# Kernel optimization log

Measured on AMD Instinct MI355X. Metric: run time of the kernel, lower is better.

## Reference

```python
import jax, jax.numpy as jnp
import numpy as np

L = 2    # num_graph_layers
T = 16   # num_tasks (batch of episodes)
N = 128  # num_samples (nodes per episode)
F = 128  # num_node_feats
BN_EPS = 1e-5


def setup_inputs() -> dict:
    key = jax.random.key(0)
    ks = jax.random.split(key, 8)
    return {
        "node_feats": jax.random.normal(ks[0], (T, N, F), dtype=jnp.float32),
        "edge_feats": jax.random.uniform(ks[1], (T, N, N, F), dtype=jnp.float32),
        # Conv3d(3->1, 1x1x1) weight+bias per layer -> 3 scalars + 1 bias
        "edge_w": (jax.random.normal(ks[2], (L, 3), dtype=jnp.float32) * 0.5),
        "edge_b": (jax.random.normal(ks[3], (L,), dtype=jnp.float32) * 0.1),
        # Conv2d(2->1, 1x1, no bias) -> 2 scalars per layer
        "comb_w": (jax.random.normal(ks[4], (L, 2), dtype=jnp.float32) * 0.5),
        # Conv1d(F->F, k=1, no bias) -> [out,in] per layer
        "node_w": (jax.random.normal(ks[5], (L, F, F), dtype=jnp.float32) / np.sqrt(F).astype(np.float32)),
        # BatchNorm1d affine params
        "bn_gamma": jnp.ones((L, F), dtype=jnp.float32),
        "bn_beta": jnp.zeros((L, F), dtype=jnp.float32),
    }


def _lrelu(x):
    return jnp.where(x >= 0, x, 0.01 * x)  # torch LeakyReLU default slope


def _sim_cal(x):
    # x: [T,N,F] -> clamped [cos_sim, 1-cos_sim]: [T,2,N,N]
    g = jnp.einsum('tnf,tmf->tnm', x, x)
    nrm = jnp.linalg.norm(x, axis=-1)              # [T,N]
    denom = nrm[:, :, None] * nrm[:, None, :] + 1e-6
    sim = (g / denom)[:, None]                     # [T,1,N,N]
    pred = jnp.concatenate([sim, 1.0 - sim], axis=1)
    return jnp.clip(pred, 0.0, 1.0)


def reference(node_feats, edge_feats, edge_w, edge_b, comb_w, node_w, bn_gamma, bn_beta):
    outs = [_sim_cal(node_feats)]
    n = node_feats.shape[1]
    diag_mask = (1.0 - jnp.eye(n, dtype=node_feats.dtype))[None, :, :, None]  # [1,N,N,1]
    for l in range(L):
        x = node_feats                                     # [T,N,F]
        # --- EdgeUpdateNetwork: Conv3d(3->1,1x1x1) over channels [x_i, x_i-x_j, edge] + tanh ---
        diff = x[:, :, None, :] - x[:, None, :, :]         # [T,N,N,F]
        xi = jnp.broadcast_to(x[:, :, None, :], diff.shape)
        e = jnp.tanh(edge_w[l, 0] * xi + edge_w[l, 1] * diff
                     + edge_w[l, 2] * edge_feats + edge_b[l])
        edge_feats = e * diag_mask                         # zero diagonal
        # --- NodeUpdateNetwork ---
        aggr = edge_feats.sum(axis=2)                      # [T,N,F]
        h = _lrelu(comb_w[l, 0] * x + comb_w[l, 1] * aggr) # Conv2d(2->1) + LeakyReLU
        y = jnp.einsum('tnf,gf->tng', h, node_w[l])        # Conv1d(F->F, k=1)
        mu = y.mean(axis=(0, 1))                           # BN over (batch, length)
        var = y.var(axis=(0, 1))
        y = (y - mu) * jax.lax.rsqrt(var + BN_EPS) * bn_gamma[l] + bn_beta[l]
        node_feats = _lrelu(y)
        outs.append(_sim_cal(node_feats))
    return tuple(outs)
```

## Files before the change

kernel.cpp:

```cpp
#include <hip/hip_runtime.h>

#define T_ 16
#define N_ 128
#define F_ 128

__device__ __forceinline__ float fast_tanh(float x) {
    float e = __expf(2.0f * x);
    return 1.0f - __fdividef(2.0f, e + 1.0f);
}

__device__ __forceinline__ float lrelu(float v) {
    return v >= 0.0f ? v : 0.01f * v;
}

__global__ void wprep(const float* __restrict__ W, float* __restrict__ WT,
                      float* __restrict__ bn, float* __restrict__ aggrG) {
    int l = blockIdx.y;
    int idx = blockIdx.x * 256 + threadIdx.x;
    int g = idx >> 7, f = idx & 127;
    WT[l * 16384 + f * 128 + g] = W[l * 16384 + idx];
    int lin = l * 16384 + idx;
    float4 z = make_float4(0.f, 0.f, 0.f, 0.f);
    ((float4*)aggrG)[lin * 2]     = z;
    ((float4*)aggrG)[lin * 2 + 1] = z;
    if (l == 0 && blockIdx.x == 0) {
        bn[threadIdx.x] = 0.0f;
        bn[256 + threadIdx.x] = 0.0f;
    }
}

template<int LAYER>
__global__ __launch_bounds__(256) void edge_k(const float* __restrict__ x0,
                                              const float* __restrict__ x1,
                                              const float* __restrict__ E,
                                              const float* __restrict__ ew,
                                              const float* __restrict__ eb,
                                              float* __restrict__ aggrG) {
    __shared__ float4 red[256];
    int b = blockIdx.x;
    int ti = b >> 1, h = b & 1;
    int t = ti >> 7, i = ti & 127;
    int tid = threadIdx.x, jl = tid >> 5, fg = tid & 31;

    const float4* xt0 = (const float4*)(x0 + (size_t)t * 16384);
    const float4* xt1 = (const float4*)(x1 + (size_t)t * 16384);
    const float4* Ei  = (const float4*)(E + (size_t)ti * 16384);

    float w02 = ew[2], b0 = eb[0];
    float c0 = ew[0] + ew[1], nw01 = -ew[1];
    float c1 = 0.f, nw11 = 0.f, w12 = 0.f, b1 = 0.f;
    if constexpr (LAYER == 1) { c1 = ew[3] + ew[4]; nw11 = -ew[4]; w12 = ew[5]; b1 = eb[1]; }

    float4 xi0 = xt0[i * 32 + fg];
    float4 xi1 = xi0;
    if constexpr (LAYER == 1) xi1 = xt1[i * 32 + fg];

    float4 a = make_float4(0.f, 0.f, 0.f, 0.f);
    int jbase = h * 64;

    float4 xj0[8], ev[8];
    float4 xj1[8];
    #pragma unroll
    for (int k = 0; k < 8; ++k) {
        int j = jbase + k * 8 + jl;
        ev[k]  = Ei[j * 32 + fg];
        xj0[k] = xt0[j * 32 + fg];
        if constexpr (LAYER == 1) xj1[k] = xt1[j * 32 + fg];
    }

    #pragma unroll
    for (int k = 0; k < 8; ++k) {
        int j = jbase + k * 8 + jl;
        float msk = (j != i) ? 1.0f : 0.0f;
        if constexpr (LAYER == 0) {
            a.x += msk * fast_tanh(fmaf(c0, xi0.x, fmaf(w02, ev[k].x, fmaf(nw01, xj0[k].x, b0))));
            a.y += msk * fast_tanh(fmaf(c0, xi0.y, fmaf(w02, ev[k].y, fmaf(nw01, xj0[k].y, b0))));
            a.z += msk * fast_tanh(fmaf(c0, xi0.z, fmaf(w02, ev[k].z, fmaf(nw01, xj0[k].z, b0))));
            a.w += msk * fast_tanh(fmaf(c0, xi0.w, fmaf(w02, ev[k].w, fmaf(nw01, xj0[k].w, b0))));
        } else {
            float e0x = fast_tanh(fmaf(c0, xi0.x, fmaf(w02, ev[k].x, fmaf(nw01, xj0[k].x, b0))));
            float e0y = fast_tanh(fmaf(c0, xi0.y, fmaf(w02, ev[k].y, fmaf(nw01, xj0[k].y, b0))));
            float e0z = fast_tanh(fmaf(c0, xi0.z, fmaf(w02, ev[k].z, fmaf(nw01, xj0[k].z, b0))));
            float e0w = fast_tanh(fmaf(c0, xi0.w, fmaf(w02, ev[k].w, fmaf(nw01, xj0[k].w, b0))));
            a.x += msk * fast_tanh(fmaf(c1, xi1.x, fmaf(w12, e0x, fmaf(nw11, xj1[k].x, b1))));
            a.y += msk * fast_tanh(fmaf(c1, xi1.y, fmaf(w12, e0y, fmaf(nw11, xj1[k].y, b1))));
            a.z += msk * fast_tanh(fmaf(c1, xi1.z, fmaf(w12, e0z, fmaf(nw11, xj1[k].z, b1))));
            a.w += msk * fast_tanh(fmaf(c1, xi1.w, fmaf(w12, e0w, fmaf(nw11, xj1[k].w, b1))));
        }
    }

    red[tid] = a;
    __syncthreads();
    if (tid < 32) {
        float4 r = red[tid];
        #pragma unroll
        for (int k = 1; k < 8; ++k) {
            float4 o = red[tid + 32 * k];
            r.x += o.x; r.y += o.y; r.z += o.z; r.w += o.w;
        }
        float* ap = aggrG + (size_t)ti * 128 + tid * 4;
        atomicAdd(ap + 0, r.x);
        atomicAdd(ap + 1, r.y);
        atomicAdd(ap + 2, r.z);
        atomicAdd(ap + 3, r.w);
    }
}

template<bool CLEAR>
__global__ __launch_bounds__(128) void node_k(const float* __restrict__ x,
                                              float* __restrict__ aggrG,
                                              const float* __restrict__ cw,
                                              const float* __restrict__ WT,
                                              float* __restrict__ y_out,
                                              float* __restrict__ bnL) {
    __shared__ float hs[8][128];
    int t = blockIdx.x, ch = blockIdx.y, g = threadIdx.x;
    float c0 = cw[0], c1 = cw[1];
    size_t base = ((size_t)t * 128 + ch * 8) * 128;
    #pragma unroll
    for (int r = 0; r < 8; ++r) {
        float xv = x[base + r * 128 + g];
        float av = aggrG[base + r * 128 + g];
        hs[r][g] = lrelu(fmaf(c0, xv, c1 * av));
        if (CLEAR) aggrG[base + r * 128 + g] = 0.0f;
    }
    __syncthreads();
    float acc[8];
    #pragma unroll
    for (int r = 0; r < 8; ++r) acc[r] = 0.0f;
    #pragma unroll 4
    for (int f = 0; f < 128; ++f) {
        float wv = WT[f * 128 + g];
        #pragma unroll
        for (int r = 0; r < 8; ++r) acc[r] = fmaf(hs[r][f], wv, acc[r]);
    }
    float s = 0.0f, ss = 0.0f;
    #pragma unroll
    for (int r = 0; r < 8; ++r) {
        y_out[base + r * 128 + g] = acc[r];
        s += acc[r];
        ss += acc[r] * acc[r];
    }
    atomicAdd(&bnL[g], s);
    atomicAdd(&bnL[128 + g], ss);
}

template<bool BN>
__global__ __launch_bounds__(256) void sim_k(const float* __restrict__ x,
                                             const float* __restrict__ bnS,
                                             const float* __restrict__ gamma,
                                             const float* __restrict__ beta,
                                             float* __restrict__ out,
                                             float* __restrict__ xout) {
    __shared__ float Xs[128][132];
    __shared__ float nrm[128];
    int t = blockIdx.x, ch = blockIdx.y;
    int tid = threadIdx.x;
    int m = tid & 127, rh = tid >> 7;
    const float* xt = x + (size_t)t * (N_ * F_);
    int fg = (tid & 31) * 4, ko = tid >> 5;

    float4 sc, sh;
    if constexpr (BN) {
        float4 s1 = *(const float4*)(bnS + fg);
        float4 s2 = *(const float4*)(bnS + 128 + fg);
        float4 ga = *(const float4*)(gamma + fg);
        float4 be = *(const float4*)(beta + fg);
        const float inv_n = 1.0f / 2048.0f;
        float mx = s1.x * inv_n, my = s1.y * inv_n, mz = s1.z * inv_n, mw = s1.w * inv_n;
        sc.x = rsqrtf(s2.x * inv_n - mx * mx + 1e-5f) * ga.x;
        sc.y = rsqrtf(s2.y * inv_n - my * my + 1e-5f) * ga.y;
        sc.z = rsqrtf(s2.z * inv_n - mz * mz + 1e-5f) * ga.z;
        sc.w = rsqrtf(s2.w * inv_n - mw * mw + 1e-5f) * ga.w;
        sh.x = be.x - mx * sc.x;
        sh.y = be.y - my * sc.y;
        sh.z = be.z - mz * sc.z;
        sh.w = be.w - mw * sc.w;
    }

    bool wout = false;
    if constexpr (BN) wout = (blockIdx.y == 0) && (xout != nullptr);
    for (int kb = 0; kb < 128; kb += 8) {
        int k = kb + ko;
        float4 v = *(const float4*)(xt + k * 128 + fg);
        if constexpr (BN) {
            v.x = lrelu(fmaf(v.x, sc.x, sh.x));
            v.y = lrelu(fmaf(v.y, sc.y, sh.y));
            v.z = lrelu(fmaf(v.z, sc.z, sh.z));
            v.w = lrelu(fmaf(v.w, sc.w, sh.w));
            if (wout) *(float4*)(xout + (size_t)t * 16384 + k * 128 + fg) = v;
        }
        *(float4*)&Xs[k][fg] = v;
    }
    __syncthreads();

    if (tid < 128) {
        float s = 0.0f;
        #pragma unroll 8
        for (int f = 0; f < 128; f += 4) {
            float4 v = *(float4*)&Xs[m][f];
            s += v.x * v.x + v.y * v.y + v.z * v.z + v.w * v.w;
        }
        nrm[m] = sqrtf(s);
    }
    __syncthreads();

    float acc[4];
    #pragma unroll
    for (int r = 0; r < 4; ++r) acc[r] = 0.0f;

    for (int fc = 0; fc < 128; fc += 32) {
        float xm[32];
        #pragma unroll
        for (int f = 0; f < 32; f += 4) {
            float4 v = *(float4*)&Xs[m][fc + f];
            xm[f] = v.x; xm[f + 1] = v.y; xm[f + 2] = v.z; xm[f + 3] = v.w;
        }
        #pragma unroll
        for (int r = 0; r < 4; ++r) {
            int n = ch * 8 + rh * 4 + r;
            #pragma unroll
            for (int f = 0; f < 32; f += 4) {
                float4 v = *(float4*)&Xs[n][fc + f];
                acc[r] = fmaf(xm[f], v.x,
                         fmaf(xm[f + 1], v.y,
                         fmaf(xm[f + 2], v.z,
                         fmaf(xm[f + 3], v.w, acc[r]))));
            }
        }
    }

    float nm = nrm[m];
    size_t ob = (size_t)t * 2 * 16384;
    #pragma unroll
    for (int r = 0; r < 4; ++r) {
        int n = ch * 8 + rh * 4 + r;
        float denom = nrm[n] * nm + 1e-6f;
        float sim = __fdividef(acc[r], denom);
        float s0 = fminf(fmaxf(sim, 0.0f), 1.0f);
        float s1 = fminf(fmaxf(1.0f - sim, 0.0f), 1.0f);
        out[ob + (size_t)n * 128 + m] = s0;
        out[ob + 16384 + (size_t)n * 128 + m] = s1;
    }
}

extern "C" void kernel_launch(void* const* d_in, const int* in_sizes, int n_in,
                              void* d_out, int out_size, void* d_ws, size_t ws_size,
                              hipStream_t stream) {
    const float* x0    = (const float*)d_in[0];
    const float* E     = (const float*)d_in[1];
    const float* ew    = (const float*)d_in[2];
    const float* eb    = (const float*)d_in[3];
    const float* cw    = (const float*)d_in[4];
    const float* nw    = (const float*)d_in[5];
    const float* gamma = (const float*)d_in[6];
    const float* beta  = (const float*)d_in[7];
    float* out = (float*)d_out;

    float* ws    = (float*)d_ws;
    float* x1    = ws;
    float* yb    = ws + 262144;
    float* aggrG = ws + 524288;
    float* bn    = ws + 786432;
    float* WT    = ws + 786944;

    wprep<<<dim3(64, 2), 256, 0, stream>>>(nw, WT, bn, aggrG);

    sim_k<false><<<dim3(16, 16), 256, 0, stream>>>(x0, nullptr, nullptr, nullptr, out, nullptr);

    edge_k<0><<<4096, 256, 0, stream>>>(x0, x0, E, ew, eb, aggrG);
    node_k<true><<<dim3(16, 16), 128, 0, stream>>>(x0, aggrG, cw, WT, yb, bn);
    sim_k<true><<<dim3(16, 16), 256, 0, stream>>>(yb, bn, gamma, beta, out + 524288, x1);

    edge_k<1><<<4096, 256, 0, stream>>>(x0, x1, E, ew, eb, aggrG);
    node_k<false><<<dim3(16, 16), 128, 0, stream>>>(x1, aggrG, cw + 2, WT + 16384, yb, bn + 256);
    sim_k<true><<<dim3(16, 16), 256, 0, stream>>>(yb, bn + 256, gamma + 128, beta + 128,
                                                  out + 1048576, nullptr);
}
```

Measured before the change: 306.6 us.

## Split edge kernel into four j-quarters with partial buffers instead of atomics

```diff
diff --git a/kernel.cpp b/kernel.cpp
--- a/kernel.cpp
+++ b/kernel.cpp
@@ -14,15 +14,11 @@
 }
 
 __global__ void wprep(const float* __restrict__ W, float* __restrict__ WT,
-                      float* __restrict__ bn, float* __restrict__ aggrG) {
+                      float* __restrict__ bn) {
     int l = blockIdx.y;
     int idx = blockIdx.x * 256 + threadIdx.x;
     int g = idx >> 7, f = idx & 127;
     WT[l * 16384 + f * 128 + g] = W[l * 16384 + idx];
-    int lin = l * 16384 + idx;
-    float4 z = make_float4(0.f, 0.f, 0.f, 0.f);
-    ((float4*)aggrG)[lin * 2]     = z;
-    ((float4*)aggrG)[lin * 2 + 1] = z;
     if (l == 0 && blockIdx.x == 0) {
         bn[threadIdx.x] = 0.0f;
         bn[256 + threadIdx.x] = 0.0f;
@@ -35,10 +31,10 @@
                                               const float* __restrict__ E,
                                               const float* __restrict__ ew,
                                               const float* __restrict__ eb,
-                                              float* __restrict__ aggrG) {
+                                              float* __restrict__ aggrP) {
     __shared__ float4 red[256];
     int b = blockIdx.x;
-    int ti = b >> 1, h = b & 1;
+    int ti = b >> 2, q = b & 3;
     int t = ti >> 7, i = ti & 127;
     int tid = threadIdx.x, jl = tid >> 5, fg = tid & 31;
 
@@ -56,12 +52,11 @@
     if constexpr (LAYER == 1) xi1 = xt1[i * 32 + fg];
 
     float4 a = make_float4(0.f, 0.f, 0.f, 0.f);
-    int jbase = h * 64;
-
-    float4 xj0[8], ev[8];
-    float4 xj1[8];
-    #pragma unroll
-    for (int k = 0; k < 8; ++k) {
+    int jbase = q * 32;
+
+    float4 xj0[4], ev[4], xj1[4];
+    #pragma unroll
+    for (int k = 0; k < 4; ++k) {
         int j = jbase + k * 8 + jl;
         ev[k]  = Ei[j * 32 + fg];
         xj0[k] = xt0[j * 32 + fg];
@@ -69,7 +64,7 @@
     }
 
     #pragma unroll
-    for (int k = 0; k < 8; ++k) {
+    for (int k = 0; k < 4; ++k) {
         int j = jbase + k * 8 + jl;
         float msk = (j != i) ? 1.0f : 0.0f;
         if constexpr (LAYER == 0) {
@@ -98,17 +93,12 @@
             float4 o = red[tid + 32 * k];
             r.x += o.x; r.y += o.y; r.z += o.z; r.w += o.w;
         }
-        float* ap = aggrG + (size_t)ti * 128 + tid * 4;
-        atomicAdd(ap + 0, r.x);
-        atomicAdd(ap + 1, r.y);
-        atomicAdd(ap + 2, r.z);
-        atomicAdd(ap + 3, r.w);
-    }
-}
-
-template<bool CLEAR>
+        ((float4*)(aggrP + (size_t)q * 262144))[ti * 32 + tid] = r;
+    }
+}
+
 __global__ __launch_bounds__(128) void node_k(const float* __restrict__ x,
-                                              float* __restrict__ aggrG,
+                                              const float* __restrict__ aggrP,
                                               const float* __restrict__ cw,
                                               const float* __restrict__ WT,
                                               float* __restrict__ y_out,
@@ -120,9 +110,11 @@
     #pragma unroll
     for (int r = 0; r < 8; ++r) {
         float xv = x[base + r * 128 + g];
-        float av = aggrG[base + r * 128 + g];
+        float av = aggrP[base + r * 128 + g]
+                 + aggrP[262144 + base + r * 128 + g]
+                 + aggrP[524288 + base + r * 128 + g]
+                 + aggrP[786432 + base + r * 128 + g];
         hs[r][g] = lrelu(fmaf(c0, xv, c1 * av));
-        if (CLEAR) aggrG[base + r * 128 + g] = 0.0f;
     }
     __syncthreads();
     float acc[8];
@@ -260,20 +252,20 @@
     float* ws    = (float*)d_ws;
     float* x1    = ws;
     float* yb    = ws + 262144;
-    float* aggrG = ws + 524288;
-    float* bn    = ws + 786432;
-    float* WT    = ws + 786944;
-
-    wprep<<<dim3(64, 2), 256, 0, stream>>>(nw, WT, bn, aggrG);
+    float* aggrP = ws + 524288;
+    float* bn    = ws + 1572864;
+    float* WT    = ws + 1573376;
+
+    wprep<<<dim3(64, 2), 256, 0, stream>>>(nw, WT, bn);
 
     sim_k<false><<<dim3(16, 16), 256, 0, stream>>>(x0, nullptr, nullptr, nullptr, out, nullptr);
 
-    edge_k<0><<<4096, 256, 0, stream>>>(x0, x0, E, ew, eb, aggrG);
-    node_k<true><<<dim3(16, 16), 128, 0, stream>>>(x0, aggrG, cw, WT, yb, bn);
+    edge_k<0><<<8192, 256, 0, stream>>>(x0, x0, E, ew, eb, aggrP);
+    node_k<<<dim3(16, 16), 128, 0, stream>>>(x0, aggrP, cw, WT, yb, bn);
     sim_k<true><<<dim3(16, 16), 256, 0, stream>>>(yb, bn, gamma, beta, out + 524288, x1);
 
-    edge_k<1><<<4096, 256, 0, stream>>>(x0, x1, E, ew, eb, aggrG);
-    node_k<false><<<dim3(16, 16), 128, 0, stream>>>(x1, aggrG, cw + 2, WT + 16384, yb, bn + 256);
+    edge_k<1><<<8192, 256, 0, stream>>>(x0, x1, E, ew, eb, aggrP);
+    node_k<<<dim3(16, 16), 128, 0, stream>>>(x1, aggrP, cw + 2, WT + 16384, yb, bn + 256);
     sim_k<true><<<dim3(16, 16), 256, 0, stream>>>(yb, bn + 256, gamma + 128, beta + 128,
                                                   out + 1048576, nullptr);
 }
```

Measured after the change: 303.1 us. About the same (-1.2%).
